# Performance work log

Measured on AMD Instinct MI355X. Metric: run time of the kernel, lower is better.

Reference implementation:

```python
import jax, jax.numpy as jnp
import numpy as np

HEADS = 16
HEAD_DIM = 64
EMB = 1024
B, S = 4, 2048
SCALE = 1.0 / 8.0  # fixed constant in the original code
MASK_PENALTY = -50.0  # original adds -50 * upper_triangular, not -inf


def setup_inputs() -> dict:
    key = jax.random.key(0)
    ks = jax.random.split(key, 5)
    x = jax.random.normal(ks[0], (B, S, EMB), dtype=jnp.float32)
    Wq = jax.random.normal(ks[1], (EMB, HEADS * HEAD_DIM), dtype=jnp.float32) * 0.02
    Wk = jax.random.normal(ks[2], (EMB, HEADS * HEAD_DIM), dtype=jnp.float32) * 0.02
    Wv = jax.random.normal(ks[3], (EMB, HEADS * HEAD_DIM), dtype=jnp.float32) * 0.02
    Wr = jax.random.normal(ks[4], (HEADS * HEAD_DIM, EMB), dtype=jnp.float32) * 0.02
    return {"x": x, "Wq": Wq, "Wk": Wk, "Wv": Wv, "Wr": Wr}


def reference(x, Wq, Wk, Wv, Wr):
    b, s, _ = x.shape
    # project and split heads: [b, s, h, d]
    q = (x @ Wq).reshape(b, s, HEADS, HEAD_DIM)
    k = (x @ Wk).reshape(b, s, HEADS, HEAD_DIM)
    v = (x @ Wv).reshape(b, s, HEADS, HEAD_DIM)
    # scores: [b, h, s, s]
    scores = SCALE * jnp.einsum('bqhd,bkhd->bhqk', q, k)
    # causal additive mask: -50 on strictly-upper triangle (faithful to original)
    causal = jnp.triu(jnp.ones((s, s), dtype=x.dtype), k=1)
    scores = scores + MASK_PENALTY * causal
    attn = jax.nn.softmax(scores, axis=-1)
    out = jnp.einsum('bhqk,bkhd->bqhd', attn, v).reshape(b, s, HEADS * HEAD_DIM)
    return out @ Wr
```

## Files before the change

kernel.cpp:

```cpp
#include <hip/hip_runtime.h>

typedef _Float16 f16;
typedef _Float16 f16x8 __attribute__((ext_vector_type(8)));
typedef _Float16 f16x4 __attribute__((ext_vector_type(4)));
typedef float f32x4 __attribute__((ext_vector_type(4)));

#define MFMA16(A, B, C) __builtin_amdgcn_mfma_f32_16x16x32_f16((A), (B), (C), 0, 0, 0)

__device__ __forceinline__ void async16(void* lds, const void* gp) {
    __builtin_amdgcn_global_load_lds(
        (__attribute__((address_space(1))) void*)(gp),
        (__attribute__((address_space(3))) void*)(lds), 16, 0, 0);
}

__global__ __launch_bounds__(256) void k_convert(const float* __restrict__ in,
                                                 f16* __restrict__ out, int n) {
    int i = (blockIdx.x * 256 + threadIdx.x) * 4;
    if (i + 3 < n) {
        float4 v = *(const float4*)(in + i);
        f16x4 o = {(f16)v.x, (f16)v.y, (f16)v.z, (f16)v.w};
        *(f16x4*)(out + i) = o;
    }
}

__global__ __launch_bounds__(256) void k_transpose_w4(const float* __restrict__ Wq,
                                                      const float* __restrict__ Wk,
                                                      const float* __restrict__ Wv,
                                                      const float* __restrict__ Wr,
                                                      f16* __restrict__ Wqkvt,
                                                      f16* __restrict__ Wrt) {
    __shared__ float tile[32][33];
    int z = blockIdx.z;
    const float* W = (z == 0) ? Wq : (z == 1) ? Wk : (z == 2) ? Wv : Wr;
    f16* Wt = (z == 3) ? Wrt : Wqkvt + z * 1048576;
    int c0 = blockIdx.x * 32, r0 = blockIdx.y * 32;
    int tx = threadIdx.x, ty = threadIdx.y;
#pragma unroll
    for (int j = 0; j < 32; j += 8)
        tile[ty + j][tx] = W[(r0 + ty + j) * 1024 + c0 + tx];
    __syncthreads();
#pragma unroll
    for (int j = 0; j < 32; j += 8)
        Wt[(c0 + ty + j) * 1024 + r0 + tx] = (f16)tile[tx][ty + j];
}

__global__ __launch_bounds__(256) void k_transpose_v(const f16* __restrict__ QKV,
                                                     f16* __restrict__ Vt) {
    __shared__ f16 tile[32][33];
    int s0 = blockIdx.x * 32;
    int d0 = blockIdx.y * 32;
    int bh = blockIdx.z;
    int b = bh >> 4, h = bh & 15;
    int tx = threadIdx.x, ty = threadIdx.y;
#pragma unroll
    for (int j = 0; j < 32; j += 8)
        tile[ty + j][tx] = QKV[(b * 2048 + s0 + ty + j) * 3072 + 2048 + h * 64 + d0 + tx];
    __syncthreads();
#pragma unroll
    for (int j = 0; j < 32; j += 8)
        Vt[(bh * 64 + d0 + ty + j) * 2048 + s0 + tx] = tile[tx][ty + j];
}

template <bool OUT_F16>
__global__ __launch_bounds__(256) void k_gemm_bt(const f16* __restrict__ A,
                                                 const f16* __restrict__ Bt,
                                                 void* __restrict__ Cv,
                                                 int M, int N, int K) {
    __shared__ f16 As[128][32];
    __shared__ f16 Bs[128][32];
    int t = threadIdx.x;
    int lane = t & 63, w = t >> 6;
    int wm = (w >> 1) * 64, wn = (w & 1) * 64;
    int m0 = blockIdx.y * 128, n0 = blockIdx.x * 128;
    int ln = lane & 15, g = lane >> 4;

    int lin0 = w * 128 + lane, lin1 = lin0 + 64;
    int r0 = lin0 >> 2, c0 = (lin0 & 3) ^ ((r0 >> 1) & 3);
    int r1 = lin1 >> 2, c1 = (lin1 & 3) ^ ((r1 >> 1) & 3);
    const f16* gA0 = A + (size_t)(m0 + r0) * K + c0 * 8;
    const f16* gA1 = A + (size_t)(m0 + r1) * K + c1 * 8;
    const f16* gB0 = Bt + (size_t)(n0 + r0) * K + c0 * 8;
    const f16* gB1 = Bt + (size_t)(n0 + r1) * K + c1 * 8;
    f16* lA0 = &As[0][0] + w * 1024;
    f16* lB0 = &Bs[0][0] + w * 1024;

    f32x4 acc[4][4] = {};
    int sw = (ln >> 1) & 3;

    for (int k0 = 0; k0 < K; k0 += 32) {
        __syncthreads();
        async16(lA0, gA0 + k0);
        async16(lA0 + 512, gA1 + k0);
        async16(lB0, gB0 + k0);
        async16(lB0 + 512, gB1 + k0);
        __syncthreads();
        f16x8 af[4], bf[4];
#pragma unroll
        for (int i = 0; i < 4; i++) {
            af[i] = *(const f16x8*)&As[wm + i * 16 + ln][(g ^ sw) * 8];
            bf[i] = *(const f16x8*)&Bs[wn + i * 16 + ln][(g ^ sw) * 8];
        }
#pragma unroll
        for (int mt = 0; mt < 4; mt++)
#pragma unroll
            for (int nt = 0; nt < 4; nt++)
                acc[mt][nt] = MFMA16(af[mt], bf[nt], acc[mt][nt]);
    }

    int rg = g * 4;
#pragma unroll
    for (int mt = 0; mt < 4; mt++)
#pragma unroll
        for (int nt = 0; nt < 4; nt++)
#pragma unroll
            for (int r = 0; r < 4; r++) {
                int row = m0 + wm + mt * 16 + rg + r;
                int col = n0 + wn + nt * 16 + ln;
                float v = acc[mt][nt][r];
                if (OUT_F16)
                    ((f16*)Cv)[(size_t)row * N + col] = (f16)v;
                else
                    ((float*)Cv)[(size_t)row * N + col] = v;
            }
}

__global__ __launch_bounds__(256, 2) void k_attn(const f16* __restrict__ QKV,
                                                 const f16* __restrict__ Vt,
                                                 f16* __restrict__ Ob) {
    __shared__ f16 Ks[2][64][72];
    __shared__ f16 Vs[2][64][72];
    int bh = blockIdx.x, qt = blockIdx.y;
    int b = bh >> 4, h = bh & 15;
    int t = threadIdx.x, lane = t & 63, wq = t >> 6;
    int ln = lane & 15, g = lane >> 4, g8 = g * 8, rg = g * 4;

    int kr0 = t >> 3, kc0 = (t & 7) * 8;
    int kr1 = kr0 + 32;
    int kg0 = ((kr0 & 16) >> 2) | ((kr0 & 12) << 1) | (kr0 & 3);
    int kg1 = kg0 + 32;
    const f16* Kbase = QKV + (size_t)b * 2048 * 3072 + 1024 + h * 64;
    const f16* Vbase = Vt + (size_t)bh * 64 * 2048;

    const float C_SCL = 0.18033688f;
    const float C_MSK = -72.134752f;
    f16x8 ones;
#pragma unroll
    for (int j = 0; j < 8; j++) ones[j] = (f16)1.f;

    int q0 = qt * 128;
    int nk = 2 * qt + 2;

    int4 rk0, rk1, rv0, rv1;
#define LOADT(j)                                                          \
    do {                                                                  \
        size_t kO = (size_t)(j) * 64;                                     \
        rk0 = *(const int4*)(Kbase + (kO + kg0) * 3072 + kc0);            \
        rk1 = *(const int4*)(Kbase + (kO + kg1) * 3072 + kc0);            \
        rv0 = *(const int4*)(Vbase + (size_t)kr0 * 2048 + kO + kc0);      \
        rv1 = *(const int4*)(Vbase + (size_t)kr1 * 2048 + kO + kc0);      \
    } while (0)
#define STORET(bi)                                                        \
    do {                                                                  \
        *(int4*)&Ks[bi][kr0][kc0] = rk0;                                  \
        *(int4*)&Ks[bi][kr1][kc0] = rk1;                                  \
        *(int4*)&Vs[bi][kr0][kc0] = rv0;                                  \
        *(int4*)&Vs[bi][kr1][kc0] = rv1;                                  \
    } while (0)

    LOADT(0);
    STORET(0);
    LOADT(1);
    __syncthreads();

    f16x8 bq[2][2];
#pragma unroll
    for (int nt = 0; nt < 2; nt++)
#pragma unroll
        for (int kd = 0; kd < 2; kd++)
            bq[nt][kd] = *(const f16x8*)(QKV +
                (size_t)(b * 2048 + q0 + wq * 32 + nt * 16 + ln) * 3072 +
                h * 64 + kd * 32 + g8);

    f32x4 oacc[2][4] = {};
    f32x4 osum[2] = {};

    for (int kt = 0; kt < nk; kt++) {
        int cur = kt & 1;
        int k0 = kt * 64;
        bool active = (k0 <= q0 + wq * 32 + 31);

        f16x8 ak[2][4];
        if (active) {
#pragma unroll
            for (int kd = 0; kd < 2; kd++)
#pragma unroll
                for (int mt = 0; mt < 4; mt++)
                    ak[kd][mt] = *(const f16x8*)&Ks[cur][mt * 16 + ln][kd * 32 + g8];
        }
        if (kt + 1 < nk) STORET(cur ^ 1);
        if (kt + 2 < nk) LOADT(kt + 2);

        if (active) {
            f32x4 sacc[4][2] = {};
#pragma unroll
            for (int kd = 0; kd < 2; kd++)
#pragma unroll
                for (int mt = 0; mt < 4; mt++)
#pragma unroll
                    for (int nt = 0; nt < 2; nt++)
                        sacc[mt][nt] = MFMA16(ak[kd][mt], bq[nt][kd], sacc[mt][nt]);

            bool needs_mask = (k0 + 63 > q0 + wq * 32);
            f16x8 ap[2][2];
#pragma unroll
            for (int nt = 0; nt < 2; nt++) {
                int q = q0 + wq * 32 + nt * 16 + ln;
#pragma unroll
                for (int mt = 0; mt < 4; mt++) {
                    int kb = mt >> 1, hi4 = (mt & 1) * 4;
#pragma unroll
                    for (int r = 0; r < 4; r++) {
                        float e;
                        if (needs_mask) {
                            int kk = k0 + kb * 32 + hi4 + 8 * g + r;
                            e = __builtin_amdgcn_exp2f(
                                fmaf(sacc[mt][nt][r], C_SCL, (kk > q) ? C_MSK : 0.f));
                        } else {
                            e = __builtin_amdgcn_exp2f(sacc[mt][nt][r] * C_SCL);
                        }
                        ap[nt][kb][hi4 + r] = (f16)e;
                    }
                }
            }

#pragma unroll
            for (int kk = 0; kk < 2; kk++) {
                f16x8 bv[4];
#pragma unroll
                for (int dt = 0; dt < 4; dt++)
                    bv[dt] = *(const f16x8*)&Vs[cur][dt * 16 + ln][kk * 32 + g8];
#pragma unroll
                for (int nt = 0; nt < 2; nt++) {
#pragma unroll
                    for (int dt = 0; dt < 4; dt++)
                        oacc[nt][dt] = MFMA16(ap[nt][kk], bv[dt], oacc[nt][dt]);
                    osum[nt] = MFMA16(ap[nt][kk], ones, osum[nt]);
                }
            }
        }
        __syncthreads();
    }

#pragma unroll
    for (int nt = 0; nt < 2; nt++)
#pragma unroll
        for (int r = 0; r < 4; r++) {
            float inv = __builtin_amdgcn_rcpf(osum[nt][r]);
            int row = b * 2048 + q0 + wq * 32 + nt * 16 + rg + r;
#pragma unroll
            for (int dt = 0; dt < 4; dt++)
                Ob[(size_t)row * 1024 + h * 64 + dt * 16 + ln] =
                    (f16)(oacc[nt][dt][r] * inv);
        }
#undef LOADT
#undef STORET
}

extern "C" void kernel_launch(void* const* d_in, const int* in_sizes, int n_in,
                              void* d_out, int out_size, void* d_ws, size_t ws_size,
                              hipStream_t stream) {
    const float* x = (const float*)d_in[0];
    const float* Wq = (const float*)d_in[1];
    const float* Wk = (const float*)d_in[2];
    const float* Wv = (const float*)d_in[3];
    const float* Wr = (const float*)d_in[4];
    float* out = (float*)d_out;

    f16* ws = (f16*)d_ws;
    f16* xb    = ws;
    f16* Wqkvt = xb + 8388608;
    f16* Wrt   = Wqkvt + 3145728;
    f16* QKVb  = Wrt + 1048576;
    f16* Vtb   = QKVb + 25165824;
    f16* Obuf  = Vtb + 8388608;

    k_convert<<<8192, 256, 0, stream>>>(x, xb, 8388608);
    dim3 tb(32, 8);
    k_transpose_w4<<<dim3(32, 32, 4), tb, 0, stream>>>(Wq, Wk, Wv, Wr, Wqkvt, Wrt);
    k_gemm_bt<true><<<dim3(24, 64), 256, 0, stream>>>(xb, Wqkvt, QKVb, 8192, 3072, 1024);
    k_transpose_v<<<dim3(64, 2, 64), tb, 0, stream>>>(QKVb, Vtb);
    k_attn<<<dim3(64, 16), 256, 0, stream>>>(QKVb, Vtb, Obuf);
    k_gemm_bt<false><<<dim3(8, 64), 256, 0, stream>>>(Obuf, Wrt, out, 8192, 1024, 1024);
}
```

Measured before the change: 297.2 us.

## Balance causal attention work by pairing query tiles, with a split-K merge

Each attention block now handles two query tiles. In the first phase it covers the leading key tiles of the long tile 15-pi, and in the second phase the trailing key tiles of the short tile pi, so every block processes 17 key tiles instead of between 2 and 32. Each block writes its partial normalized outputs and row sums to a workspace, and a new merge kernel combines the two parts per query tile by weighting them with their row sums. This removes the tail imbalance of the causal grid. The cost is an extra kernel launch and a partial-output buffer that must be written and read back.

```diff
diff --git a/kernel.cpp b/kernel.cpp
--- a/kernel.cpp
+++ b/kernel.cpp
@@ -126,10 +126,11 @@
 
 __global__ __launch_bounds__(256, 2) void k_attn(const f16* __restrict__ QKV,
                                                  const f16* __restrict__ Vt,
-                                                 f16* __restrict__ Ob) {
+                                                 f16* __restrict__ Opart,
+                                                 float* __restrict__ Rsum) {
     __shared__ f16 Ks[2][64][72];
     __shared__ f16 Vs[2][64][72];
-    int bh = blockIdx.x, qt = blockIdx.y;
+    int bh = blockIdx.x, pi = blockIdx.y;
     int b = bh >> 4, h = bh & 15;
     int t = threadIdx.x, lane = t & 63, wq = t >> 6;
     int ln = lane & 15, g = lane >> 4, g8 = g * 8, rg = g * 4;
@@ -147,13 +148,14 @@
 #pragma unroll
     for (int j = 0; j < 8; j++) ones[j] = (f16)1.f;
 
-    int q0 = qt * 128;
-    int nk = 2 * qt + 2;
+    int nk0 = 16 - pi;
 
     int4 rk0, rk1, rv0, rv1;
 #define LOADT(j)                                                          \
     do {                                                                  \
-        size_t kO = (size_t)(j) * 64;                                     \
+        int j_ = (j);                                                     \
+        int kt_ = (j_ < nk0) ? j_ : j_ - nk0 + pi + 1;                    \
+        size_t kO = (size_t)kt_ * 64;                                     \
         rk0 = *(const int4*)(Kbase + (kO + kg0) * 3072 + kc0);            \
         rk1 = *(const int4*)(Kbase + (kO + kg1) * 3072 + kc0);            \
         rv0 = *(const int4*)(Vbase + (size_t)kr0 * 2048 + kO + kc0);      \
@@ -172,98 +174,130 @@
     LOADT(1);
     __syncthreads();
 
-    f16x8 bq[2][2];
-#pragma unroll
-    for (int nt = 0; nt < 2; nt++)
-#pragma unroll
-        for (int kd = 0; kd < 2; kd++)
-            bq[nt][kd] = *(const f16x8*)(QKV +
-                (size_t)(b * 2048 + q0 + wq * 32 + nt * 16 + ln) * 3072 +
-                h * 64 + kd * 32 + g8);
-
-    f32x4 oacc[2][4] = {};
-    f32x4 osum[2] = {};
-
-    for (int kt = 0; kt < nk; kt++) {
-        int cur = kt & 1;
-        int k0 = kt * 64;
-        bool active = (k0 <= q0 + wq * 32 + 31);
-
-        f16x8 ak[2][4];
-        if (active) {
+    int i = 0;
+    for (int phase = 0; phase < 2; phase++) {
+        int qt  = phase ? pi : 15 - pi;
+        int ktB = phase ? pi + 1 : 0;
+        int ktE = phase ? 2 * pi + 2 : 16 - pi;
+        int q0 = qt * 128;
+
+        f16x8 bq[2][2];
+#pragma unroll
+        for (int nt = 0; nt < 2; nt++)
 #pragma unroll
             for (int kd = 0; kd < 2; kd++)
-#pragma unroll
-                for (int mt = 0; mt < 4; mt++)
-                    ak[kd][mt] = *(const f16x8*)&Ks[cur][mt * 16 + ln][kd * 32 + g8];
-        }
-        if (kt + 1 < nk) STORET(cur ^ 1);
-        if (kt + 2 < nk) LOADT(kt + 2);
-
-        if (active) {
-            f32x4 sacc[4][2] = {};
-#pragma unroll
-            for (int kd = 0; kd < 2; kd++)
-#pragma unroll
-                for (int mt = 0; mt < 4; mt++)
-#pragma unroll
-                    for (int nt = 0; nt < 2; nt++)
-                        sacc[mt][nt] = MFMA16(ak[kd][mt], bq[nt][kd], sacc[mt][nt]);
-
-            bool needs_mask = (k0 + 63 > q0 + wq * 32);
-            f16x8 ap[2][2];
-#pragma unroll
-            for (int nt = 0; nt < 2; nt++) {
-                int q = q0 + wq * 32 + nt * 16 + ln;
-#pragma unroll
-                for (int mt = 0; mt < 4; mt++) {
-                    int kb = mt >> 1, hi4 = (mt & 1) * 4;
-#pragma unroll
-                    for (int r = 0; r < 4; r++) {
-                        float e;
-                        if (needs_mask) {
-                            int kk = k0 + kb * 32 + hi4 + 8 * g + r;
-                            e = __builtin_amdgcn_exp2f(
-                                fmaf(sacc[mt][nt][r], C_SCL, (kk > q) ? C_MSK : 0.f));
-                        } else {
-                            e = __builtin_amdgcn_exp2f(sacc[mt][nt][r] * C_SCL);
+                bq[nt][kd] = *(const f16x8*)(QKV +
+                    (size_t)(b * 2048 + q0 + wq * 32 + nt * 16 + ln) * 3072 +
+                    h * 64 + kd * 32 + g8);
+
+        f32x4 oacc[2][4] = {};
+        f32x4 osum[2] = {};
+
+        for (int kt = ktB; kt < ktE; kt++, i++) {
+            int cur = i & 1;
+            int k0 = kt * 64;
+            bool active = (k0 <= q0 + wq * 32 + 31);
+
+            f16x8 ak[2][4];
+            if (active) {
+#pragma unroll
+                for (int kd = 0; kd < 2; kd++)
+#pragma unroll
+                    for (int mt = 0; mt < 4; mt++)
+                        ak[kd][mt] = *(const f16x8*)&Ks[cur][mt * 16 + ln][kd * 32 + g8];
+            }
+            if (i + 1 < 17) STORET(cur ^ 1);
+            if (i + 2 < 17) LOADT(i + 2);
+
+            if (active) {
+                f32x4 sacc[4][2] = {};
+#pragma unroll
+                for (int kd = 0; kd < 2; kd++)
+#pragma unroll
+                    for (int mt = 0; mt < 4; mt++)
+#pragma unroll
+                        for (int nt = 0; nt < 2; nt++)
+                            sacc[mt][nt] = MFMA16(ak[kd][mt], bq[nt][kd], sacc[mt][nt]);
+
+                bool needs_mask = (k0 + 63 > q0 + wq * 32);
+                f16x8 ap[2][2];
+#pragma unroll
+                for (int nt = 0; nt < 2; nt++) {
+                    int q = q0 + wq * 32 + nt * 16 + ln;
+#pragma unroll
+                    for (int mt = 0; mt < 4; mt++) {
+                        int kb = mt >> 1, hi4 = (mt & 1) * 4;
+#pragma unroll
+                        for (int r = 0; r < 4; r++) {
+                            float e;
+                            if (needs_mask) {
+                                int kk = k0 + kb * 32 + hi4 + 8 * g + r;
+                                e = __builtin_amdgcn_exp2f(
+                                    fmaf(sacc[mt][nt][r], C_SCL, (kk > q) ? C_MSK : 0.f));
+                            } else {
+                                e = __builtin_amdgcn_exp2f(sacc[mt][nt][r] * C_SCL);
+                            }
+                            ap[nt][kb][hi4 + r] = (f16)e;
                         }
-                        ap[nt][kb][hi4 + r] = (f16)e;
+                    }
+                }
+
+#pragma unroll
+                for (int kk = 0; kk < 2; kk++) {
+                    f16x8 bv[4];
+#pragma unroll
+                    for (int dt = 0; dt < 4; dt++)
+                        bv[dt] = *(const f16x8*)&Vs[cur][dt * 16 + ln][kk * 32 + g8];
+#pragma unroll
+                    for (int nt = 0; nt < 2; nt++) {
+#pragma unroll
+                        for (int dt = 0; dt < 4; dt++)
+                            oacc[nt][dt] = MFMA16(ap[nt][kk], bv[dt], oacc[nt][dt]);
+                        osum[nt] = MFMA16(ap[nt][kk], ones, osum[nt]);
                     }
                 }
             }
-
-#pragma unroll
-            for (int kk = 0; kk < 2; kk++) {
-                f16x8 bv[4];
+            __syncthreads();
+        }
+
+        int u = (bh * 16 + qt) * 2 + phase;
+#pragma unroll
+        for (int nt = 0; nt < 2; nt++)
+#pragma unroll
+            for (int r = 0; r < 4; r++) {
+                float rs = osum[nt][r];
+                float inv = __builtin_amdgcn_rcpf(fmaxf(rs, 1e-30f));
+                int q = wq * 32 + nt * 16 + rg + r;
+                if (ln == 0) Rsum[u * 128 + q] = rs;
 #pragma unroll
                 for (int dt = 0; dt < 4; dt++)
-                    bv[dt] = *(const f16x8*)&Vs[cur][dt * 16 + ln][kk * 32 + g8];
-#pragma unroll
-                for (int nt = 0; nt < 2; nt++) {
-#pragma unroll
-                    for (int dt = 0; dt < 4; dt++)
-                        oacc[nt][dt] = MFMA16(ap[nt][kk], bv[dt], oacc[nt][dt]);
-                    osum[nt] = MFMA16(ap[nt][kk], ones, osum[nt]);
-                }
+                    Opart[(size_t)u * 8192 + q * 64 + dt * 16 + ln] =
+                        (f16)(oacc[nt][dt][r] * inv);
             }
-        }
-        __syncthreads();
     }
-
-#pragma unroll
-    for (int nt = 0; nt < 2; nt++)
-#pragma unroll
-        for (int r = 0; r < 4; r++) {
-            float inv = __builtin_amdgcn_rcpf(osum[nt][r]);
-            int row = b * 2048 + q0 + wq * 32 + nt * 16 + rg + r;
-#pragma unroll
-            for (int dt = 0; dt < 4; dt++)
-                Ob[(size_t)row * 1024 + h * 64 + dt * 16 + ln] =
-                    (f16)(oacc[nt][dt][r] * inv);
-        }
 #undef LOADT
 #undef STORET
+}
+
+__global__ __launch_bounds__(256) void k_merge(const f16* __restrict__ Op,
+                                               const float* __restrict__ Rs,
+                                               f16* __restrict__ Ob) {
+    int idx = blockIdx.x * 256 + threadIdx.x;
+    int d8 = idx & 7;
+    int q  = (idx >> 3) & 127;
+    int qt = (idx >> 10) & 15;
+    int bh = idx >> 14;
+    int b = bh >> 4, hd = bh & 15;
+    int u0 = (bh * 16 + qt) * 2;
+    float rs0 = Rs[u0 * 128 + q], rs1 = Rs[(u0 + 1) * 128 + q];
+    float inv = __builtin_amdgcn_rcpf(rs0 + rs1);
+    f16x8 o0 = *(const f16x8*)(Op + (size_t)u0 * 8192 + q * 64 + d8 * 8);
+    f16x8 o1 = *(const f16x8*)(Op + (size_t)(u0 + 1) * 8192 + q * 64 + d8 * 8);
+    f16x8 o;
+#pragma unroll
+    for (int j = 0; j < 8; j++)
+        o[j] = (f16)((rs0 * (float)o0[j] + rs1 * (float)o1[j]) * inv);
+    *(f16x8*)(Ob + (size_t)(b * 2048 + qt * 128 + q) * 1024 + hd * 64 + d8 * 8) = o;
 }
 
 extern "C" void kernel_launch(void* const* d_in, const int* in_sizes, int n_in,
@@ -283,12 +317,15 @@
     f16* QKVb  = Wrt + 1048576;
     f16* Vtb   = QKVb + 25165824;
     f16* Obuf  = Vtb + 8388608;
+    f16* Opart = Obuf + 8388608;
+    float* Rsum = (float*)(Opart + 16777216);
 
     k_convert<<<8192, 256, 0, stream>>>(x, xb, 8388608);
     dim3 tb(32, 8);
     k_transpose_w4<<<dim3(32, 32, 4), tb, 0, stream>>>(Wq, Wk, Wv, Wr, Wqkvt, Wrt);
     k_gemm_bt<true><<<dim3(24, 64), 256, 0, stream>>>(xb, Wqkvt, QKVb, 8192, 3072, 1024);
     k_transpose_v<<<dim3(64, 2, 64), tb, 0, stream>>>(QKVb, Vtb);
-    k_attn<<<dim3(64, 16), 256, 0, stream>>>(QKVb, Vtb, Obuf);
+    k_attn<<<dim3(64, 16), 256, 0, stream>>>(QKVb, Vtb, Opart, Rsum);
+    k_merge<<<4096, 256, 0, stream>>>(Opart, Rsum, Obuf);
     k_gemm_bt<false><<<dim3(8, 64), 256, 0, stream>>>(Obuf, Wrt, out, 8192, 1024, 1024);
 }
```

After: 291.8 us. No clear change (-1.8%).
